# Performance work log

Hardware: AMD Instinct MI355X
Metric: run time of the kernel (lower is better)

Reference implementation:

```python
import jax, jax.numpy as jnp
import numpy as np

N, C, R, G, K = 4096, 128, 128, 6, 16
RADIUS = 0.8
C_OUT = 64
FLAT = G * G * G * C_OUT  # 13824


def setup_inputs() -> dict:
    key = jax.random.key(0)
    ks = jax.random.split(key, 24)
    xav = lambda k, shp: (jax.random.normal(k, shp, jnp.float32)
                          * np.sqrt(2.0 / (shp[0] + shp[1])).astype(np.float32))
    # scene points in ~[-5,5]^3 so radius-0.8 balls hold ~8 points on average
    xyz = jax.random.normal(ks[0], (N, 3), jnp.float32) * 2.5
    feats = jax.random.normal(ks[1], (N, C), jnp.float32)
    ctr = jax.random.normal(ks[2], (R, 3), jnp.float32) * 2.5
    size = jax.random.uniform(ks[3], (R, 3), jnp.float32) * 3.0 + 1.0
    yaw = jax.random.uniform(ks[4], (R, 1), jnp.float32) * (2.0 * np.pi)
    rois = jnp.concatenate([ctr, size, yaw], -1)  # [R,7] (x,y,z,dx,dy,dz,ry)
    return {
        'xyz': xyz, 'feats': feats, 'rois': rois,
        'w_m1': xav(ks[5], (3 + C, C_OUT)), 'w_m2': xav(ks[6], (C_OUT, C_OUT)),
        'w_s1': xav(ks[7], (FLAT, 1024)), 'w_s2': xav(ks[8], (1024, 512)),
        'w_c1': xav(ks[9], (512, 1024)), 'w_c2': xav(ks[10], (1024, 512)),
        'w_c3': xav(ks[11], (512, 1)), 'b_c3': jnp.zeros((1,), jnp.float32),
        'w_i1': xav(ks[12], (512, 1024)), 'w_i2': xav(ks[13], (1024, 512)),
        'w_i3': xav(ks[14], (512, 1)), 'b_i3': jnp.zeros((1,), jnp.float32),
        'w_r1': xav(ks[15], (512, 1024)), 'w_r2': xav(ks[16], (1024, 512)),
        'w_r3': jax.random.normal(ks[17], (512, 7), jnp.float32) * 0.001,
        'b_r3': jnp.zeros((7,), jnp.float32),
    }


def _grid_points(rois):
    """get_dense_grid_points + rotate_points_along_z + center shift."""
    i = jnp.arange(G)
    gi, gj, gk = jnp.meshgrid(i, i, i, indexing='ij')
    dense = jnp.stack([gi, gj, gk], -1).reshape(-1, 3).astype(rois.dtype)  # [G^3,3]
    size = rois[:, 3:6]
    local = (dense[None] + 0.5) / G * size[:, None] - size[:, None] * 0.5  # [R,G^3,3]
    c, s = jnp.cos(rois[:, 6])[:, None], jnp.sin(rois[:, 6])[:, None]
    x, y, z = local[..., 0], local[..., 1], local[..., 2]
    rot = jnp.stack([x * c - y * s, x * s + y * c, z], -1)
    return rot + rois[:, None, 0:3]  # [R,G^3,3]


def reference(xyz, feats, rois, w_m1, w_m2, w_s1, w_s2,
              w_c1, w_c2, w_c3, b_c3, w_i1, w_i2, w_i3, b_i3,
              w_r1, w_r2, w_r3, b_r3):
    gp = _grid_points(rois).reshape(-1, 3)  # [M,3], M = R*G^3
    M = gp.shape[0]
    # ball query: first K point indices within RADIUS of each grid point
    d2 = jnp.sum((gp[:, None, :] - xyz[None, :, :]) ** 2, -1)  # [M,N]
    cand = jnp.where(d2 < RADIUS * RADIUS, jnp.arange(N), N)  # invalid -> N
    neg_top, _ = jax.lax.top_k(-cand, K)
    idx = -neg_top  # K smallest candidate indices, ascending-ish
    valid = idx < N
    first = idx[:, :1]
    idx = jnp.where(valid, idx, first)  # pad with first hit (pointnet2 semantics)
    empty = ~valid[:, 0]  # balls with zero neighbors
    idx = jnp.where(empty[:, None], 0, idx)
    # group: relative xyz + point features
    rel = xyz[idx] - gp[:, None, :]               # [M,K,3]
    g = jnp.concatenate([rel, feats[idx]], -1)    # [M,K,3+C]
    # shared per-point MLP (Conv2d 1x1 + identity-init BN + ReLU)
    h = jax.nn.relu(g @ w_m1)
    h = jax.nn.relu(h @ w_m2)                     # [M,K,C_OUT]
    pooled = jnp.max(h, axis=1)                   # max_pool over neighbors
    pooled = jnp.where(empty[:, None], 0.0, pooled)
    flat = pooled.reshape(rois.shape[0], -1)      # [R, G^3*C_OUT]
    # shared FC (Conv1d k=1 stacks) then cls / iou / reg heads
    sfc = jax.nn.relu(jax.nn.relu(flat @ w_s1) @ w_s2)
    head = lambda x, w1, w2, w3, b3: jax.nn.relu(jax.nn.relu(x @ w1) @ w2) @ w3 + b3
    cls = head(sfc, w_c1, w_c2, w_c3, b_c3)   # [R,1]
    iou = head(sfc, w_i1, w_i2, w_i3, b_i3)   # [R,1]
    reg = head(sfc, w_r1, w_r2, w_r3, b_r3)   # [R,7]
    return jnp.concatenate([cls, iou, reg], -1)  # [R,9]
```

## Files before the change

kernel.cpp:

```cpp
#include <hip/hip_runtime.h>

typedef float  f32x4  __attribute__((ext_vector_type(4)));
typedef __bf16 bf16x8 __attribute__((ext_vector_type(8)));
typedef unsigned short ushort_t;

#define N_PTS 4096
#define R_ROIS 128
#define M_GP  27648
#define LDS_FENCE() asm volatile("s_waitcnt lgkmcnt(0)" ::: "memory")

static constexpr size_t OFF_GP     = 0;
static constexpr size_t OFF_PH     = 331776;
static constexpr size_t OFF_PL     = 3870720;
static constexpr size_t OFF_H1H    = 331776;
static constexpr size_t OFF_H1L    = 1118208;
static constexpr size_t OFF_H2S    = 1904640;
static constexpr size_t OFF_PART   = 7409664;
static constexpr size_t OFF_CAND   = OFF_PART;
static constexpr size_t OFF_F      = 9506816;
static constexpr size_t OFF_XYZ4   = 10555392;
static constexpr size_t OFF_NCAND  = 11603968;
static constexpr size_t OFF_W1TH   = 11604480;
static constexpr size_t OFF_W1TL   = 11625984;
static constexpr size_t OFF_W2TH   = 11647488;
static constexpr size_t OFF_W2TL   = 11656704;
static constexpr size_t OFF_FHI    = 11665920;
static constexpr size_t OFF_FLO    = 12714496;
static constexpr size_t OFF_T1H    = 11665920;
static constexpr size_t OFF_T1L    = 11928064;
static constexpr size_t OFF_SFCH   = 12190208;
static constexpr size_t OFF_SFCL   = 12321280;

static __device__ inline ushort_t f2bf(float f) {
    unsigned int u = __float_as_uint(f);
    unsigned int r = u + 0x7FFFu + ((u >> 16) & 1u);
    return (ushort_t)(r >> 16);
}
static __device__ inline float bf2f(ushort_t h) {
    return __uint_as_float(((unsigned int)h) << 16);
}
static __device__ inline ushort_t bfbits(__bf16 h) {
    return __builtin_bit_cast(ushort_t, h);
}

__global__ __launch_bounds__(256) void prep_all_k(
    const float* __restrict__ rois, const float* __restrict__ xyz,
    const float* __restrict__ feats, const float* __restrict__ w1,
    const float* __restrict__ w2, float* __restrict__ gp,
    ushort_t* __restrict__ fhi, ushort_t* __restrict__ flo,
    ushort_t* __restrict__ w1th, ushort_t* __restrict__ w1tl,
    ushort_t* __restrict__ w2th, ushort_t* __restrict__ w2tl,
    float4* __restrict__ xyz4,
    int* __restrict__ cand, int* __restrict__ ncand) {
    int b = blockIdx.x, tid = threadIdx.x;
    if (b < 108) {
        int m = b * 256 + tid;
        int r = m / 216, t = m % 216;
        int gi = t / 36, gj = (t / 6) % 6, gk = t % 6;
        const float* roi = rois + r * 7;
        float sx = roi[3], sy = roi[4], sz = roi[5];
        float lx = ((float)gi + 0.5f) / 6.0f * sx - sx * 0.5f;
        float ly = ((float)gj + 0.5f) / 6.0f * sy - sy * 0.5f;
        float lz = ((float)gk + 0.5f) / 6.0f * sz - sz * 0.5f;
        float c = cosf(roi[6]), s = sinf(roi[6]);
        gp[m * 3 + 0] = lx * c - ly * s + roi[0];
        gp[m * 3 + 1] = lx * s + ly * c + roi[1];
        gp[m * 3 + 2] = lz + roi[2];
    } else if (b < 150) {
        int t = (b - 108) * 256 + tid;
        {
            int col = t / 168, p = t % 168;
            float v = (p < 128) ? w1[(3 + p) * 64 + col]
                    : (p < 131) ? w1[(p - 128) * 64 + col] : 0.f;
            ushort_t hi = f2bf(v);
            w1th[t] = hi;
            w1tl[t] = f2bf(v - bf2f(hi));
        }
        if (t < 4608) {
            int col = t / 72, k = t % 72;
            float v = (k < 64) ? w2[k * 64 + col] : 0.f;
            ushort_t hi = f2bf(v);
            w2th[t] = hi;
            w2tl[t] = f2bf(v - bf2f(hi));
        }
    } else if (b < 2198) {
        int i = (b - 150) * 256 + tid;
        float v = feats[i];
        __bf16 h = (__bf16)v;
        fhi[i] = bfbits(h);
        flo[i] = bfbits((__bf16)(v - (float)h));
    } else if (b < 2214) {
        int i = (b - 2198) * 256 + tid;
        xyz4[i] = make_float4(xyz[i * 3 + 0], xyz[i * 3 + 1], xyz[i * 3 + 2], 0.f);
    } else {
        int r = (b - 2214) * 4 + (tid >> 6);
        int lane = tid & 63;
        const float* roi = rois + r * 7;
        float cx = roi[0], cy = roi[1], cz = roi[2];
        float sx = roi[3], sy = roi[4], sz = roi[5];
        float Rc = 0.8f + 0.4166667f * sqrtf(sx * sx + sy * sy + sz * sz) + 0.01f;
        float Rc2 = Rc * Rc;
        int* cl = cand + (size_t)r * N_PTS;
        int cnt = 0;
        for (int base = 0; base < N_PTS; base += 64) {
            int i = base + lane;
            float dx = xyz[i * 3 + 0] - cx;
            float dy = xyz[i * 3 + 1] - cy;
            float dz = xyz[i * 3 + 2] - cz;
            bool in = dx * dx + dy * dy + dz * dz < Rc2;
            unsigned long long ball = __ballot(in);
            int before = __popcll(ball & ((1ull << lane) - 1ull));
            if (in) cl[cnt + before] = i;
            cnt += __popcll(ball);
        }
        if (lane == 0) ncand[r] = cnt;
    }
}

__global__ __launch_bounds__(256) void f_gemm_k(
    const ushort_t* __restrict__ fhi, const ushort_t* __restrict__ flo,
    const ushort_t* __restrict__ w1th, const ushort_t* __restrict__ w1tl,
    float* __restrict__ F) {
    int tid = threadIdx.x;
    int w = tid >> 6, lane = tid & 63;
    int row = lane & 15, grp = lane >> 4;
    int m0 = blockIdx.x * 64 + w * 16;

    f32x4 acc[4];
#pragma unroll
    for (int nt = 0; nt < 4; nt++) acc[nt] = {0.f, 0.f, 0.f, 0.f};

#pragma unroll
    for (int ks = 0; ks < 4; ks++) {
        size_t ao = (size_t)(m0 + row) * 128 + ks * 32 + grp * 8;
        bf16x8 ah = *(const bf16x8*)&fhi[ao];
        bf16x8 al = *(const bf16x8*)&flo[ao];
#pragma unroll
        for (int nt = 0; nt < 4; nt++) {
            int bo = (nt * 16 + row) * 168 + ks * 32 + grp * 8;
            bf16x8 bh = *(const bf16x8*)&w1th[bo];
            bf16x8 bl = *(const bf16x8*)&w1tl[bo];
            acc[nt] = __builtin_amdgcn_mfma_f32_16x16x32_bf16(ah, bh, acc[nt], 0, 0, 0);
            acc[nt] = __builtin_amdgcn_mfma_f32_16x16x32_bf16(al, bh, acc[nt], 0, 0, 0);
            acc[nt] = __builtin_amdgcn_mfma_f32_16x16x32_bf16(ah, bl, acc[nt], 0, 0, 0);
        }
    }
#pragma unroll
    for (int nt = 0; nt < 4; nt++)
#pragma unroll
        for (int reg = 0; reg < 4; reg++)
            F[(size_t)(m0 + grp * 4 + reg) * 64 + nt * 16 + row] = acc[nt][reg];
}

__global__ __launch_bounds__(64) void grid_pool_v5_k(
    const float4* __restrict__ xyz4, const float* __restrict__ F,
    const float* __restrict__ gp, const int* __restrict__ cand,
    const int* __restrict__ ncand, const float* __restrict__ w_m1,
    const ushort_t* __restrict__ w2th, const ushort_t* __restrict__ w2tl,
    ushort_t* __restrict__ Afh, ushort_t* __restrict__ Afl) {
    __shared__ int s_idx[4][16];
    int lane = threadIdx.x;
    const float R2 = (float)(0.8 * 0.8);
    int row = lane & 15, grp = lane >> 4;
    int m0 = blockIdx.x * 4;
    int r = m0 / 216;

    float gxv[4], gyv[4], gzv[4];
#pragma unroll
    for (int g = 0; g < 4; g++) {
        int m = m0 + g;
        gxv[g] = gp[m * 3 + 0];
        gyv[g] = gp[m * 3 + 1];
        gzv[g] = gp[m * 3 + 2];
    }

    int nc = ncand[r];
    const int* cl = cand + (size_t)r * N_PTS;
    int cnt0 = 0, cnt1 = 0, cnt2 = 0, cnt3 = 0;
    for (int base = 0; base < nc; base += 64) {
        int t = base + lane;
        float px = 1e30f, py = 1e30f, pz = 1e30f;
        int i = 0;
        if (t < nc) {
            i = cl[t];
            float4 p = xyz4[i];
            px = p.x; py = p.y; pz = p.z;
        }
#pragma unroll
        for (int g = 0; g < 4; g++) {
            float dx = px - gxv[g], dy = py - gyv[g], dz = pz - gzv[g];
            bool in = dx * dx + dy * dy + dz * dz < R2;
            unsigned long long ball = __ballot(in);
            int before = __popcll(ball & ((1ull << lane) - 1ull));
            int cnt = (g == 0) ? cnt0 : (g == 1) ? cnt1 : (g == 2) ? cnt2 : cnt3;
            int pos = cnt + before;
            if (in && pos < 16) s_idx[g][pos] = i;
            int add = __popcll(ball);
            if (g == 0) cnt0 += add; else if (g == 1) cnt1 += add;
            else if (g == 2) cnt2 += add; else cnt3 += add;
        }
        if (cnt0 >= 16 && cnt1 >= 16 && cnt2 >= 16 && cnt3 >= 16) break;
    }
    LDS_FENCE();

    bool empty[4];
#pragma unroll
    for (int g = 0; g < 4; g++) {
        int cnt = (g == 0) ? cnt0 : (g == 1) ? cnt1 : (g == 2) ? cnt2 : cnt3;
        int c = min(cnt, 16);
        empty[g] = (c == 0);
        if (lane == 0) {
            if (c == 0) {
                for (int p = 0; p < 16; p++) s_idx[g][p] = 0;
            } else {
                int f = s_idx[g][0];
                for (int p = c; p < 16; p++) s_idx[g][p] = f;
            }
        }
    }
    LDS_FENCE();

    int pi[4];
    float rx[4], ry[4], rz[4];
#pragma unroll
    for (int g = 0; g < 4; g++) {
        pi[g] = s_idx[g][row];
        float4 p = xyz4[pi[g]];
        rx[g] = p.x - gxv[g];
        ry[g] = p.y - gyv[g];
        rz[g] = p.z - gzv[g];
    }

    f32x4 p[4][4];
#pragma unroll
    for (int g = 0; g < 4; g++)
#pragma unroll
        for (int nt = 0; nt < 4; nt++) p[g][nt] = {0.f, 0.f, 0.f, 0.f};

#pragma unroll
    for (int ks = 0; ks < 2; ks++) {
        float w1r0[8], w1r1[8], w1r2[8];
        {
            const float* wp = w_m1 + ks * 32 + grp * 8;
            *(float4*)&w1r0[0] = *(const float4*)(wp);
            *(float4*)&w1r0[4] = *(const float4*)(wp + 4);
            *(float4*)&w1r1[0] = *(const float4*)(wp + 64);
            *(float4*)&w1r1[4] = *(const float4*)(wp + 68);
            *(float4*)&w1r2[0] = *(const float4*)(wp + 128);
            *(float4*)&w1r2[4] = *(const float4*)(wp + 132);
        }
        bf16x8 zah[4], zal[4];
#pragma unroll
        for (int g = 0; g < 4; g++) {
            const float* Fr = F + (size_t)pi[g] * 64 + ks * 32 + grp * 8;
            float fv[8];
            *(float4*)&fv[0] = *(const float4*)Fr;
            *(float4*)&fv[4] = *(const float4*)(Fr + 4);
            bf16x8 hh, ll;
#pragma unroll
            for (int j = 0; j < 8; j++) {
                float zv = fv[j] + rx[g] * w1r0[j] + ry[g] * w1r1[j] + rz[g] * w1r2[j];
                float v = fmaxf(zv, 0.f);
                __bf16 h = (__bf16)v;
                hh[j] = h;
                ll[j] = (__bf16)(v - (float)h);
            }
            zah[g] = hh; zal[g] = ll;
        }
#pragma unroll
        for (int nt = 0; nt < 4; nt++) {
            int bo = (nt * 16 + row) * 72 + ks * 32 + grp * 8;
            bf16x8 bh = *(const bf16x8*)&w2th[bo];
            bf16x8 bl = *(const bf16x8*)&w2tl[bo];
#pragma unroll
            for (int g = 0; g < 4; g++) {
                p[g][nt] = __builtin_amdgcn_mfma_f32_16x16x32_bf16(zah[g], bh, p[g][nt], 0, 0, 0);
                p[g][nt] = __builtin_amdgcn_mfma_f32_16x16x32_bf16(zal[g], bh, p[g][nt], 0, 0, 0);
                p[g][nt] = __builtin_amdgcn_mfma_f32_16x16x32_bf16(zah[g], bl, p[g][nt], 0, 0, 0);
            }
        }
    }

#pragma unroll
    for (int g = 0; g < 4; g++) {
        int m = m0 + g;
        int t = m % 216;
#pragma unroll
        for (int nt = 0; nt < 4; nt++) {
            float mv = fmaxf(fmaxf(fmaxf(p[g][nt][0], p[g][nt][1]),
                                   fmaxf(p[g][nt][2], p[g][nt][3])), 0.f);
            mv = fmaxf(mv, __shfl_xor(mv, 16));
            mv = fmaxf(mv, __shfl_xor(mv, 32));
            if (grp == 0) {
                float v = empty[g] ? 0.f : mv;
                __bf16 h = (__bf16)v;
                int kt = t * 2 + (nt >> 1);
                size_t o = ((size_t)kt * 128 + r) * 32 + (nt & 1) * 16 + row;
                Afh[o] = bfbits(h);
                Afl[o] = bfbits((__bf16)(v - (float)h));
            }
        }
    }
}

__global__ __launch_bounds__(256) void gemm_stream_k(
    const ushort_t* __restrict__ A_h, const ushort_t* __restrict__ A_l,
    size_t a_stride,
    const float* __restrict__ B0, const float* __restrict__ B1,
    const float* __restrict__ B2,
    float* __restrict__ P, int N, int Kt, int S) {
    __shared__ __attribute__((aligned(16))) ushort_t Bs_h[32][40];
    __shared__ __attribute__((aligned(16))) ushort_t Bs_l[32][40];
    int tid = threadIdx.x;
    int w = tid >> 6, lane = tid & 63;
    int row = lane & 15, grp = lane >> 4;
    int z = blockIdx.z, head = z / S, s = z % S;
    int n0 = blockIdx.x * 32, m0 = blockIdx.y * 64;
    const float* B = (head == 0) ? B0 : (head == 1) ? B1 : B2;
    const ushort_t* Ah = A_h + (size_t)head * a_stride;
    const ushort_t* Al = A_l + (size_t)head * a_stride;
    const int STEPS = Kt / (32 * S);
    int kt0 = s * STEPS;
    int nl = tid & 31, kg = tid >> 5;

    f32x4 acc0 = {0.f, 0.f, 0.f, 0.f};
    f32x4 acc1 = {0.f, 0.f, 0.f, 0.f};
    int arow = m0 + w * 16 + row;
    const float* bbase = B + ((size_t)kt0 * 32 + kg * 4) * N + n0 + nl;
    size_t abase = ((size_t)kt0 * 128 + arow) * 32 + grp * 8;

#define LOADB(t, dst)                                                         \
    do {                                                                      \
        const float* bp_ = bbase + (size_t)(t) * 32 * N;                      \
        dst.x = bp_[0];                                                       \
        dst.y = bp_[(size_t)N];                                               \
        dst.z = bp_[(size_t)2 * N];                                           \
        dst.w = bp_[(size_t)3 * N];                                           \
    } while (0)
#define LOADA(t, dh, dl)                                                      \
    do {                                                                      \
        size_t ao_ = abase + (size_t)(t) * 4096;                              \
        dh = *(const bf16x8*)&Ah[ao_];                                        \
        dl = *(const bf16x8*)&Al[ao_];                                        \
    } while (0)
#define STAGE(bv)                                                             \
    do {                                                                      \
        ushort_t hs0 = f2bf(bv.x), ls0;                                       \
        ls0 = f2bf(bv.x - bf2f(hs0));                                         \
        ushort_t hs1 = f2bf(bv.y), ls1;                                       \
        ls1 = f2bf(bv.y - bf2f(hs1));                                         \
        ushort_t hs2 = f2bf(bv.z), ls2;                                       \
        ls2 = f2bf(bv.z - bf2f(hs2));                                         \
        ushort_t hs3 = f2bf(bv.w), ls3;                                       \
        ls3 = f2bf(bv.w - bf2f(hs3));                                         \
        uint2 hw_ = make_uint2((unsigned)hs0 | ((unsigned)hs1 << 16),         \
                               (unsigned)hs2 | ((unsigned)hs3 << 16));        \
        uint2 lw_ = make_uint2((unsigned)ls0 | ((unsigned)ls1 << 16),         \
                               (unsigned)ls2 | ((unsigned)ls3 << 16));        \
        *(uint2*)&Bs_h[nl][kg * 4] = hw_;                                     \
        *(uint2*)&Bs_l[nl][kg * 4] = lw_;                                     \
    } while (0)
#define COMPUTE(ah_, al_)                                                     \
    do {                                                                      \
        bf16x8 bh0 = *(const bf16x8*)&Bs_h[row][grp * 8];                     \
        bf16x8 bl0 = *(const bf16x8*)&Bs_l[row][grp * 8];                     \
        acc0 = __builtin_amdgcn_mfma_f32_16x16x32_bf16(ah_, bh0, acc0, 0, 0, 0); \
        acc0 = __builtin_amdgcn_mfma_f32_16x16x32_bf16(al_, bh0, acc0, 0, 0, 0); \
        acc0 = __builtin_amdgcn_mfma_f32_16x16x32_bf16(ah_, bl0, acc0, 0, 0, 0); \
        bf16x8 bh1 = *(const bf16x8*)&Bs_h[16 + row][grp * 8];                \
        bf16x8 bl1 = *(const bf16x8*)&Bs_l[16 + row][grp * 8];                \
        acc1 = __builtin_amdgcn_mfma_f32_16x16x32_bf16(ah_, bh1, acc1, 0, 0, 0); \
        acc1 = __builtin_amdgcn_mfma_f32_16x16x32_bf16(al_, bh1, acc1, 0, 0, 0); \
        acc1 = __builtin_amdgcn_mfma_f32_16x16x32_bf16(ah_, bl1, acc1, 0, 0, 0); \
    } while (0)

    float4 bv0, bv1;
    bf16x8 a0h, a0l, a1h, a1l;
    LOADB(0, bv0);
    LOADA(0, a0h, a0l);
    LOADB(1, bv1);
    LOADA(1, a1h, a1l);

    for (int t = 0; t < STEPS; t += 2) {
        STAGE(bv0);
        __syncthreads();
        COMPUTE(a0h, a0l);
        if (t + 2 < STEPS) {
            LOADB(t + 2, bv0);
            LOADA(t + 2, a0h, a0l);
        }
        __syncthreads();
        STAGE(bv1);
        __syncthreads();
        COMPUTE(a1h, a1l);
        if (t + 3 < STEPS) {
            LOADB(t + 3, bv1);
            LOADA(t + 3, a1h, a1l);
        }
        __syncthreads();
    }
#undef LOADB
#undef LOADA
#undef STAGE
#undef COMPUTE

    size_t pb = (size_t)z * 128 * N;
#pragma unroll
    for (int reg = 0; reg < 4; reg++) {
        int mrow = m0 + w * 16 + grp * 4 + reg;
        P[pb + (size_t)mrow * N + n0 + row] = acc0[reg];
        P[pb + (size_t)mrow * N + n0 + 16 + row] = acc1[reg];
    }
}

__global__ __launch_bounds__(256) void reduce_frag_k(
    const float* __restrict__ P, ushort_t* __restrict__ C_h,
    ushort_t* __restrict__ C_l, float* __restrict__ C_f, int out_f32,
    int MNper, int S, int heads, int Nn) {
    int i = blockIdx.x * 256 + threadIdx.x;
    if (i >= heads * MNper) return;
    int h = i / MNper, j = i % MNper;
    float v = 0.f;
    for (int s = 0; s < S; s++) v += P[((size_t)(h * S + s)) * MNper + j];
    v = fmaxf(v, 0.f);
    if (out_f32) {
        C_f[i] = v;
        return;
    }
    int m = j / Nn, n = j % Nn;
    size_t off = (size_t)h * MNper + ((size_t)(n >> 5) * 128 + m) * 32 + (n & 31);
    __bf16 hh = (__bf16)v;
    C_h[off] = bfbits(hh);
    C_l[off] = bfbits((__bf16)(v - (float)hh));
}

__global__ __launch_bounds__(256) void head_out3_k(
    const float* __restrict__ h2s, const float* __restrict__ w_c3,
    const float* __restrict__ w_i3, const float* __restrict__ w_r3,
    const float* __restrict__ b_c3, const float* __restrict__ b_i3,
    const float* __restrict__ b_r3, float* __restrict__ out) {
    int t = blockIdx.x * 256 + threadIdx.x;
    if (t >= 128 * 9) return;
    int r = t / 9, col = t % 9;
    int head = (col == 0) ? 0 : (col == 1) ? 1 : 2;
    int p = (col < 2) ? 0 : col - 2;
    int Pn = (head == 2) ? 7 : 1;
    const float* h2 = h2s + (size_t)head * (128 * 512) + (size_t)r * 512;
    const float* w3 = (head == 0) ? w_c3 : (head == 1) ? w_i3 : w_r3;
    float acc = ((head == 0) ? b_c3 : (head == 1) ? b_i3 : b_r3)[p];
    for (int j = 0; j < 512; j++) acc += h2[j] * w3[j * Pn + p];
    out[r * 9 + col] = acc;
}

extern "C" void kernel_launch(void* const* d_in, const int* in_sizes, int n_in,
                              void* d_out, int out_size, void* d_ws, size_t ws_size,
                              hipStream_t stream) {
    const float* xyz   = (const float*)d_in[0];
    const float* feats = (const float*)d_in[1];
    const float* rois  = (const float*)d_in[2];
    const float* w_m1  = (const float*)d_in[3];
    const float* w_m2  = (const float*)d_in[4];
    const float* w_s1  = (const float*)d_in[5];
    const float* w_s2  = (const float*)d_in[6];
    const float* w_c1  = (const float*)d_in[7];
    const float* w_c2  = (const float*)d_in[8];
    const float* w_c3  = (const float*)d_in[9];
    const float* b_c3  = (const float*)d_in[10];
    const float* w_i1  = (const float*)d_in[11];
    const float* w_i2  = (const float*)d_in[12];
    const float* w_i3  = (const float*)d_in[13];
    const float* b_i3  = (const float*)d_in[14];
    const float* w_r1  = (const float*)d_in[15];
    const float* w_r2  = (const float*)d_in[16];
    const float* w_r3  = (const float*)d_in[17];
    const float* b_r3  = (const float*)d_in[18];
    float* out = (float*)d_out;

    char* ws = (char*)d_ws;
    float*    gp     = (float*)(ws + OFF_GP);
    ushort_t* afh    = (ushort_t*)(ws + OFF_PH);
    ushort_t* afl    = (ushort_t*)(ws + OFF_PL);
    float*    part   = (float*)(ws + OFF_PART);
    int*      cand   = (int*)(ws + OFF_CAND);
    float*    F      = (float*)(ws + OFF_F);
    float4*   xyz4   = (float4*)(ws + OFF_XYZ4);
    int*      ncand  = (int*)(ws + OFF_NCAND);
    ushort_t* w1th   = (ushort_t*)(ws + OFF_W1TH);
    ushort_t* w1tl   = (ushort_t*)(ws + OFF_W1TL);
    ushort_t* w2th   = (ushort_t*)(ws + OFF_W2TH);
    ushort_t* w2tl   = (ushort_t*)(ws + OFF_W2TL);
    ushort_t* fhi    = (ushort_t*)(ws + OFF_FHI);
    ushort_t* flo    = (ushort_t*)(ws + OFF_FLO);
    ushort_t* t1h    = (ushort_t*)(ws + OFF_T1H);
    ushort_t* t1l    = (ushort_t*)(ws + OFF_T1L);
    ushort_t* sfch   = (ushort_t*)(ws + OFF_SFCH);
    ushort_t* sfcl   = (ushort_t*)(ws + OFF_SFCL);
    ushort_t* h1h    = (ushort_t*)(ws + OFF_H1H);
    ushort_t* h1l    = (ushort_t*)(ws + OFF_H1L);
    float*    h2s    = (float*)(ws + OFF_H2S);

    hipLaunchKernelGGL(prep_all_k, dim3(2246), dim3(256), 0, stream,
                       rois, xyz, feats, w_m1, w_m2, gp, fhi, flo,
                       w1th, w1tl, w2th, w2tl, xyz4, cand, ncand);
    hipLaunchKernelGGL(f_gemm_k, dim3(64), dim3(256), 0, stream,
                       fhi, flo, w1th, w1tl, F);
    hipLaunchKernelGGL(grid_pool_v5_k, dim3(M_GP / 4), dim3(64), 0, stream,
                       xyz4, F, gp, cand, ncand, w_m1, w2th, w2tl, afh, afl);
    hipLaunchKernelGGL(gemm_stream_k, dim3(32, 2, 8), dim3(256), 0, stream,
                       afh, afl, (size_t)0, w_s1, w_s1, w_s1, part, 1024, 13824, 8);
    hipLaunchKernelGGL(reduce_frag_k, dim3(512), dim3(256), 0, stream,
                       part, t1h, t1l, (float*)nullptr, 0, 128 * 1024, 8, 1, 1024);
    hipLaunchKernelGGL(gemm_stream_k, dim3(16, 2, 8), dim3(256), 0, stream,
                       t1h, t1l, (size_t)0, w_s2, w_s2, w_s2, part, 512, 1024, 8);
    hipLaunchKernelGGL(reduce_frag_k, dim3(256), dim3(256), 0, stream,
                       part, sfch, sfcl, (float*)nullptr, 0, 128 * 512, 8, 1, 512);
    hipLaunchKernelGGL(gemm_stream_k, dim3(32, 2, 6), dim3(256), 0, stream,
                       sfch, sfcl, (size_t)0, w_c1, w_i1, w_r1, part, 1024, 512, 2);
    hipLaunchKernelGGL(reduce_frag_k, dim3(1536), dim3(256), 0, stream,
                       part, h1h, h1l, (float*)nullptr, 0, 128 * 1024, 2, 3, 1024);
    hipLaunchKernelGGL(gemm_stream_k, dim3(16, 2, 12), dim3(256), 0, stream,
                       h1h, h1l, (size_t)131072, w_c2, w_i2, w_r2, part, 512, 1024, 4);
    hipLaunchKernelGGL(reduce_frag_k, dim3(768), dim3(256), 0, stream,
                       part, (ushort_t*)nullptr, (ushort_t*)nullptr, h2s, 1,
                       128 * 512, 4, 3, 512);
    hipLaunchKernelGGL(head_out3_k, dim3(5), dim3(256), 0, stream,
                       h2s, w_c3, w_i3, w_r3, b_c3, b_i3, b_r3, out);
}
```

Before: 167.3 us.

## Split ball query into per-ROI search kernel separate from grouped MLP

The fused grid-pool kernel is split in two. A new search kernel runs one 256-thread block per ROI, with one thread per grid point scanning the ROI's candidate list serially, and writes 16 neighbor indices per grid point to workspace. The MLP kernel then reads those indices instead of doing the wave-wide ballot search itself. This removes the ballot/popcount search from the MFMA kernel and gives each thread its own early exit, at the cost of an extra launch, an index buffer round trip, and only 128 blocks for the search phase, which may underfill the GPU. The index buffer reuses the FHI region, which f_gemm has already consumed by the time it is written.

Result: slower. 290.7 us (+73.7%).

```diff
diff --git a/kernel.cpp b/kernel.cpp
--- a/kernel.cpp
+++ b/kernel.cpp
@@ -26,6 +26,7 @@
 static constexpr size_t OFF_W2TL   = 11656704;
 static constexpr size_t OFF_FHI    = 11665920;
 static constexpr size_t OFF_FLO    = 12714496;
+static constexpr size_t OFF_IDX    = 11665920;
 static constexpr size_t OFF_T1H    = 11665920;
 static constexpr size_t OFF_T1L    = 11928064;
 static constexpr size_t OFF_SFCH   = 12190208;
@@ -152,83 +153,88 @@
             F[(size_t)(m0 + grp * 4 + reg) * 64 + nt * 16 + row] = acc[nt][reg];
 }
 
-__global__ __launch_bounds__(64) void grid_pool_v5_k(
+__global__ __launch_bounds__(256) void search_k(
+    const float4* __restrict__ xyz4, const float* __restrict__ gp,
+    const int* __restrict__ cand, const int* __restrict__ ncand,
+    int* __restrict__ idxout) {
+    __shared__ int s_list[216][16];
+    int t = threadIdx.x, r = blockIdx.x;
+    bool active = t < 216;
+    int m = r * 216 + t;
+    float gx = 0.f, gy = 0.f, gz = 0.f;
+    if (active) {
+        gx = gp[m * 3 + 0];
+        gy = gp[m * 3 + 1];
+        gz = gp[m * 3 + 2];
+    }
+    int cnt = active ? 0 : 16;
+    int nc = ncand[r];
+    const int* cl = cand + (size_t)r * N_PTS;
+    const float R2 = (float)(0.8 * 0.8);
+
+    for (int j0 = 0; j0 < nc; j0 += 4) {
+        int i0 = cl[j0] & 4095;
+        int i1 = cl[j0 + 1] & 4095;
+        int i2 = cl[j0 + 2] & 4095;
+        int i3 = cl[j0 + 3] & 4095;
+        float4 p0 = xyz4[i0];
+        float4 p1 = xyz4[i1];
+        float4 p2 = xyz4[i2];
+        float4 p3 = xyz4[i3];
+#define TESTC(jj, ii, pp)                                                     \
+        do {                                                                  \
+            float dx = pp.x - gx, dy = pp.y - gy, dz = pp.z - gz;             \
+            bool in = active && ((jj) < nc) &&                                \
+                      (dx * dx + dy * dy + dz * dz < R2);                     \
+            if (in && cnt < 16) s_list[t][cnt] = (ii);                        \
+            cnt += in ? 1 : 0;                                                \
+        } while (0)
+        TESTC(j0, i0, p0);
+        TESTC(j0 + 1, i1, p1);
+        TESTC(j0 + 2, i2, p2);
+        TESTC(j0 + 3, i3, p3);
+#undef TESTC
+        if (__all(cnt >= 16)) break;
+    }
+    if (active) {
+        int c = min(cnt, 16);
+        if (c == 0) {
+#pragma unroll
+            for (int p = 0; p < 16; p++) s_list[t][p] = -1;
+        } else {
+            int f = s_list[t][0];
+            for (int p = c; p < 16; p++) s_list[t][p] = f;
+        }
+        int4* dst = (int4*)(idxout + (size_t)m * 16);
+#pragma unroll
+        for (int q = 0; q < 4; q++) dst[q] = *(int4*)&s_list[t][q * 4];
+    }
+}
+
+__global__ __launch_bounds__(64) void mlp_k(
     const float4* __restrict__ xyz4, const float* __restrict__ F,
-    const float* __restrict__ gp, const int* __restrict__ cand,
-    const int* __restrict__ ncand, const float* __restrict__ w_m1,
+    const float* __restrict__ gp, const int* __restrict__ idx,
+    const float* __restrict__ w_m1,
     const ushort_t* __restrict__ w2th, const ushort_t* __restrict__ w2tl,
     ushort_t* __restrict__ Afh, ushort_t* __restrict__ Afl) {
-    __shared__ int s_idx[4][16];
     int lane = threadIdx.x;
-    const float R2 = (float)(0.8 * 0.8);
     int row = lane & 15, grp = lane >> 4;
     int m0 = blockIdx.x * 4;
     int r = m0 / 216;
 
-    float gxv[4], gyv[4], gzv[4];
+    int pi[4];
+    bool empty[4];
+    float rx[4], ry[4], rz[4];
 #pragma unroll
     for (int g = 0; g < 4; g++) {
         int m = m0 + g;
-        gxv[g] = gp[m * 3 + 0];
-        gyv[g] = gp[m * 3 + 1];
-        gzv[g] = gp[m * 3 + 2];
-    }
-
-    int nc = ncand[r];
-    const int* cl = cand + (size_t)r * N_PTS;
-    int cnt0 = 0, cnt1 = 0, cnt2 = 0, cnt3 = 0;
-    for (int base = 0; base < nc; base += 64) {
-        int t = base + lane;
-        float px = 1e30f, py = 1e30f, pz = 1e30f;
-        int i = 0;
-        if (t < nc) {
-            i = cl[t];
-            float4 p = xyz4[i];
-            px = p.x; py = p.y; pz = p.z;
-        }
-#pragma unroll
-        for (int g = 0; g < 4; g++) {
-            float dx = px - gxv[g], dy = py - gyv[g], dz = pz - gzv[g];
-            bool in = dx * dx + dy * dy + dz * dz < R2;
-            unsigned long long ball = __ballot(in);
-            int before = __popcll(ball & ((1ull << lane) - 1ull));
-            int cnt = (g == 0) ? cnt0 : (g == 1) ? cnt1 : (g == 2) ? cnt2 : cnt3;
-            int pos = cnt + before;
-            if (in && pos < 16) s_idx[g][pos] = i;
-            int add = __popcll(ball);
-            if (g == 0) cnt0 += add; else if (g == 1) cnt1 += add;
-            else if (g == 2) cnt2 += add; else cnt3 += add;
-        }
-        if (cnt0 >= 16 && cnt1 >= 16 && cnt2 >= 16 && cnt3 >= 16) break;
-    }
-    LDS_FENCE();
-
-    bool empty[4];
-#pragma unroll
-    for (int g = 0; g < 4; g++) {
-        int cnt = (g == 0) ? cnt0 : (g == 1) ? cnt1 : (g == 2) ? cnt2 : cnt3;
-        int c = min(cnt, 16);
-        empty[g] = (c == 0);
-        if (lane == 0) {
-            if (c == 0) {
-                for (int p = 0; p < 16; p++) s_idx[g][p] = 0;
-            } else {
-                int f = s_idx[g][0];
-                for (int p = c; p < 16; p++) s_idx[g][p] = f;
-            }
-        }
-    }
-    LDS_FENCE();
-
-    int pi[4];
-    float rx[4], ry[4], rz[4];
-#pragma unroll
-    for (int g = 0; g < 4; g++) {
-        pi[g] = s_idx[g][row];
+        int iv = idx[(size_t)m * 16 + row];
+        empty[g] = (iv < 0);
+        pi[g] = empty[g] ? 0 : iv;
         float4 p = xyz4[pi[g]];
-        rx[g] = p.x - gxv[g];
-        ry[g] = p.y - gyv[g];
-        rz[g] = p.z - gzv[g];
+        rx[g] = p.x - gp[m * 3 + 0];
+        ry[g] = p.y - gp[m * 3 + 1];
+        rz[g] = p.z - gp[m * 3 + 2];
     }
 
     f32x4 p[4][4];
@@ -491,6 +497,7 @@
     ushort_t* w2tl   = (ushort_t*)(ws + OFF_W2TL);
     ushort_t* fhi    = (ushort_t*)(ws + OFF_FHI);
     ushort_t* flo    = (ushort_t*)(ws + OFF_FLO);
+    int*      idx    = (int*)(ws + OFF_IDX);
     ushort_t* t1h    = (ushort_t*)(ws + OFF_T1H);
     ushort_t* t1l    = (ushort_t*)(ws + OFF_T1L);
     ushort_t* sfch   = (ushort_t*)(ws + OFF_SFCH);
@@ -504,8 +511,10 @@
                        w1th, w1tl, w2th, w2tl, xyz4, cand, ncand);
     hipLaunchKernelGGL(f_gemm_k, dim3(64), dim3(256), 0, stream,
                        fhi, flo, w1th, w1tl, F);
-    hipLaunchKernelGGL(grid_pool_v5_k, dim3(M_GP / 4), dim3(64), 0, stream,
-                       xyz4, F, gp, cand, ncand, w_m1, w2th, w2tl, afh, afl);
+    hipLaunchKernelGGL(search_k, dim3(R_ROIS), dim3(256), 0, stream,
+                       xyz4, gp, cand, ncand, idx);
+    hipLaunchKernelGGL(mlp_k, dim3(M_GP / 4), dim3(64), 0, stream,
+                       xyz4, F, gp, idx, w_m1, w2th, w2tl, afh, afl);
     hipLaunchKernelGGL(gemm_stream_k, dim3(32, 2, 8), dim3(256), 0, stream,
                        afh, afl, (size_t)0, w_s1, w_s1, w_s1, part, 1024, 13824, 8);
     hipLaunchKernelGGL(reduce_frag_k, dim3(512), dim3(256), 0, stream,
```

## Split grid ball-query scan and per-point MLP into separate kernels

Applied to the files above, without the earlier changes.

The fused grid pooling kernel is split in two. A scan kernel does the radius ball query and writes 16 neighbor indices per grid point to workspace, with -1 marking an empty ball. An MLP kernel then reads those indices and runs the MFMA MLP and max-pool. Both kernels use 256-thread blocks holding four independent waves instead of 64-thread blocks. The aim is to separate the divergent, latency-bound scan from the MFMA-heavy MLP so each can be scheduled well, at the cost of an extra launch and an index round-trip through memory.

Measured after the change: 169.1 us. About the same (+1.1%).

```diff
diff --git a/kernel.cpp b/kernel.cpp
--- a/kernel.cpp
+++ b/kernel.cpp
@@ -26,6 +26,7 @@
 static constexpr size_t OFF_W2TL   = 11656704;
 static constexpr size_t OFF_FHI    = 11665920;
 static constexpr size_t OFF_FLO    = 12714496;
+static constexpr size_t OFF_IDX    = 11665920;
 static constexpr size_t OFF_T1H    = 11665920;
 static constexpr size_t OFF_T1L    = 11928064;
 static constexpr size_t OFF_SFCH   = 12190208;
@@ -152,17 +153,15 @@
             F[(size_t)(m0 + grp * 4 + reg) * 64 + nt * 16 + row] = acc[nt][reg];
 }
 
-__global__ __launch_bounds__(64) void grid_pool_v5_k(
-    const float4* __restrict__ xyz4, const float* __restrict__ F,
-    const float* __restrict__ gp, const int* __restrict__ cand,
-    const int* __restrict__ ncand, const float* __restrict__ w_m1,
-    const ushort_t* __restrict__ w2th, const ushort_t* __restrict__ w2tl,
-    ushort_t* __restrict__ Afh, ushort_t* __restrict__ Afl) {
-    __shared__ int s_idx[4][16];
-    int lane = threadIdx.x;
+__global__ __launch_bounds__(256) void scan_k(
+    const float4* __restrict__ xyz4, const float* __restrict__ gp,
+    const int* __restrict__ cand, const int* __restrict__ ncand,
+    int* __restrict__ idxout) {
+    __shared__ int s_idx[4][4][16];
+    int tid = threadIdx.x;
+    int w = tid >> 6, lane = tid & 63;
     const float R2 = (float)(0.8 * 0.8);
-    int row = lane & 15, grp = lane >> 4;
-    int m0 = blockIdx.x * 4;
+    int m0 = (blockIdx.x * 4 + w) * 4;
     int r = m0 / 216;
 
     float gxv[4], gyv[4], gzv[4];
@@ -194,7 +193,7 @@
             int before = __popcll(ball & ((1ull << lane) - 1ull));
             int cnt = (g == 0) ? cnt0 : (g == 1) ? cnt1 : (g == 2) ? cnt2 : cnt3;
             int pos = cnt + before;
-            if (in && pos < 16) s_idx[g][pos] = i;
+            if (in && pos < 16) s_idx[w][g][pos] = i;
             int add = __popcll(ball);
             if (g == 0) cnt0 += add; else if (g == 1) cnt1 += add;
             else if (g == 2) cnt2 += add; else cnt3 += add;
@@ -203,32 +202,48 @@
     }
     LDS_FENCE();
 
-    bool empty[4];
 #pragma unroll
     for (int g = 0; g < 4; g++) {
         int cnt = (g == 0) ? cnt0 : (g == 1) ? cnt1 : (g == 2) ? cnt2 : cnt3;
         int c = min(cnt, 16);
-        empty[g] = (c == 0);
-        if (lane == 0) {
+        if (lane < 16) {
+            int v;
             if (c == 0) {
-                for (int p = 0; p < 16; p++) s_idx[g][p] = 0;
+                v = -1;
             } else {
-                int f = s_idx[g][0];
-                for (int p = c; p < 16; p++) s_idx[g][p] = f;
+                int f = s_idx[w][g][0];
+                v = (lane < c) ? s_idx[w][g][lane] : f;
             }
-        }
-    }
-    LDS_FENCE();
+            idxout[(size_t)(m0 + g) * 16 + lane] = v;
+        }
+    }
+}
+
+__global__ __launch_bounds__(256) void mlp_k(
+    const float4* __restrict__ xyz4, const float* __restrict__ F,
+    const float* __restrict__ gp, const int* __restrict__ idx,
+    const float* __restrict__ w_m1,
+    const ushort_t* __restrict__ w2th, const ushort_t* __restrict__ w2tl,
+    ushort_t* __restrict__ Afh, ushort_t* __restrict__ Afl) {
+    int tid = threadIdx.x;
+    int w = tid >> 6, lane = tid & 63;
+    int row = lane & 15, grp = lane >> 4;
+    int m0 = (blockIdx.x * 4 + w) * 4;
+    int r = m0 / 216;
 
     int pi[4];
+    bool empty[4];
     float rx[4], ry[4], rz[4];
 #pragma unroll
     for (int g = 0; g < 4; g++) {
-        pi[g] = s_idx[g][row];
+        int m = m0 + g;
+        int iv = idx[(size_t)m * 16 + row];
+        empty[g] = (iv < 0);
+        pi[g] = empty[g] ? 0 : iv;
         float4 p = xyz4[pi[g]];
-        rx[g] = p.x - gxv[g];
-        ry[g] = p.y - gyv[g];
-        rz[g] = p.z - gzv[g];
+        rx[g] = p.x - gp[m * 3 + 0];
+        ry[g] = p.y - gp[m * 3 + 1];
+        rz[g] = p.z - gp[m * 3 + 2];
     }
 
     f32x4 p[4][4];
@@ -491,6 +506,7 @@
     ushort_t* w2tl   = (ushort_t*)(ws + OFF_W2TL);
     ushort_t* fhi    = (ushort_t*)(ws + OFF_FHI);
     ushort_t* flo    = (ushort_t*)(ws + OFF_FLO);
+    int*      idx    = (int*)(ws + OFF_IDX);
     ushort_t* t1h    = (ushort_t*)(ws + OFF_T1H);
     ushort_t* t1l    = (ushort_t*)(ws + OFF_T1L);
     ushort_t* sfch   = (ushort_t*)(ws + OFF_SFCH);
@@ -504,8 +520,10 @@
                        w1th, w1tl, w2th, w2tl, xyz4, cand, ncand);
     hipLaunchKernelGGL(f_gemm_k, dim3(64), dim3(256), 0, stream,
                        fhi, flo, w1th, w1tl, F);
-    hipLaunchKernelGGL(grid_pool_v5_k, dim3(M_GP / 4), dim3(64), 0, stream,
-                       xyz4, F, gp, cand, ncand, w_m1, w2th, w2tl, afh, afl);
+    hipLaunchKernelGGL(scan_k, dim3(M_GP / 16), dim3(256), 0, stream,
+                       xyz4, gp, cand, ncand, idx);
+    hipLaunchKernelGGL(mlp_k, dim3(M_GP / 16), dim3(256), 0, stream,
+                       xyz4, F, gp, idx, w_m1, w2th, w2tl, afh, afl);
     hipLaunchKernelGGL(gemm_stream_k, dim3(32, 2, 8), dim3(256), 0, stream,
                        afh, afl, (size_t)0, w_s1, w_s1, w_s1, part, 1024, 13824, 8);
     hipLaunchKernelGGL(reduce_frag_k, dim3(512), dim3(256), 0, stream,
```
